# Kernel optimization log

Measured on AMD Instinct MI355X. Metric: run time of the kernel, lower is better.

The kernel has to match this reference:

```python
import jax, jax.numpy as jnp
import numpy as np

NUM_HEADS = 16
HEAD_DIM = 64  # hidden_size // num_heads


def _logsparse_allowed(seq_len):
    # allowed[i, j] True if key j is attended by query i:
    # j == i, j == i-1, or j == i - 2^k (k >= 1); combined with causal (j <= i).
    i = jnp.arange(seq_len)[:, None]
    j = jnp.arange(seq_len)[None, :]
    diff = i - j
    pow2 = (diff > 0) & ((diff & (diff - 1)) == 0)  # covers diff==1 and diff==2^k
    return (diff == 0) | pow2  # implies diff >= 0, so causal is subsumed


def setup_inputs() -> dict:
    key = jax.random.key(0)
    ks = jax.random.split(key, 7)
    B, S, H = 4, 2048, 1024
    return {
        "hidden_states": jax.random.normal(ks[0], (B, S, H), dtype=jnp.float32),
        "attention_mask": jnp.zeros((B, 1, 1, S), dtype=jnp.float32),
        "Wq": jax.random.normal(ks[1], (H, H), dtype=jnp.float32) * 0.02,
        "bq": jnp.zeros((H,), dtype=jnp.float32),
        "Wk": jax.random.normal(ks[2], (H, H), dtype=jnp.float32) * 0.02,
        "bk": jnp.zeros((H,), dtype=jnp.float32),
        "Wv": jax.random.normal(ks[3], (H, H), dtype=jnp.float32) * 0.02,
        "bv": jnp.zeros((H,), dtype=jnp.float32),
    }


def _split_heads(x):
    B, S, _ = x.shape
    return x.reshape(B, S, NUM_HEADS, HEAD_DIM).transpose(0, 2, 1, 3)  # b h t d


def reference(hidden_states, attention_mask, Wq, bq, Wk, bk, Wv, bv):
    B, S, H = hidden_states.shape
    q = _split_heads(hidden_states @ Wq.T + bq)
    k = _split_heads(hidden_states @ Wk.T + bk)
    v = _split_heads(hidden_states @ Wv.T + bv)

    scores = jnp.einsum("bhqd,bhkd->bhqk", q, k) * (HEAD_DIM ** -0.5)
    allowed = _logsparse_allowed(S)  # [S, S] bool
    scores = jnp.where(allowed[None, None], scores, -jnp.inf)
    scores = scores + attention_mask  # [B,1,1,S] additive mask
    probs = jax.nn.softmax(scores, axis=-1)
    out = jnp.einsum("bhqk,bhkd->bhqd", probs, v)
    return out.transpose(0, 2, 1, 3).reshape(B, S, H)
```

## Files before the change

kernel.cpp:

```cpp
#include <hip/hip_runtime.h>
#include <hip/hip_bf16.h>

#define S_LEN   2048
#define NHEADS  16
#define HDIM    64
#define HID     1024
#define BATCH   4
#define M_ROWS  (BATCH * S_LEN)

typedef __attribute__((ext_vector_type(8))) short short8;
typedef __attribute__((ext_vector_type(4))) float floatx4;
typedef __attribute__((ext_vector_type(4))) unsigned short ushort4v;

__device__ __forceinline__ unsigned short f2bf_rne(float x) {
  union { float f; unsigned u; } v; v.f = x;
  unsigned r = v.u + 0x7fffu + ((v.u >> 16) & 1u);
  return (unsigned short)(r >> 16);
}

__device__ __forceinline__ float bf2f(unsigned short u) {
  union { unsigned u; float f; } c; c.u = ((unsigned)u) << 16;
  return c.f;
}

__device__ __forceinline__ void glds16(const unsigned short* g, unsigned short* l) {
  __builtin_amdgcn_global_load_lds(
      (const __attribute__((address_space(1))) unsigned int*)g,
      (__attribute__((address_space(3))) unsigned int*)l, 16, 0, 0);
}

#define HS4 (M_ROWS * HID / 4)
#define W4  (HID * HID / 4)
__global__ __launch_bounds__(256) void cast_all(
    const float* __restrict__ hs, const float* __restrict__ Wq,
    const float* __restrict__ Wk, const float* __restrict__ Wv,
    unsigned short* __restrict__ hsb, unsigned short* __restrict__ wqb,
    unsigned short* __restrict__ wkb, unsigned short* __restrict__ wvb) {
  int idx = blockIdx.x * 256 + threadIdx.x;
  const float* in;
  unsigned short* out;
  int off;
  if (idx < HS4) {
    in = hs; out = hsb; off = idx;
  } else {
    int r = idx - HS4;
    int seg = r >> 18;
    off = r & (W4 - 1);
    in  = (seg == 0) ? Wq  : (seg == 1) ? Wk  : Wv;
    out = (seg == 0) ? wqb : (seg == 1) ? wkb : wvb;
  }
  floatx4 v = __builtin_nontemporal_load((const floatx4*)in + off);
  ushort4v o;
  o.x = f2bf_rne(v.x);
  o.y = f2bf_rne(v.y);
  o.z = f2bf_rne(v.z);
  o.w = f2bf_rne(v.w);
  ((ushort4v*)out)[off] = o;
}

__global__ __launch_bounds__(512, 2) void qkv_gemm(
    const unsigned short* __restrict__ A,
    const unsigned short* __restrict__ W0, const unsigned short* __restrict__ W1,
    const unsigned short* __restrict__ W2,
    const float* __restrict__ b0, const float* __restrict__ b1,
    const float* __restrict__ b2,
    unsigned short* __restrict__ O0, unsigned short* __restrict__ O1,
    unsigned short* __restrict__ O2) {
  const int K = HID;
  const int N = HID;

  __shared__ __align__(16) unsigned short lds[3 * 24576];

  const int tid = threadIdx.x;
  const int w = tid >> 6;
  const int lane = tid & 63;

  const int bid = blockIdx.x;
  const int xcd = bid & 7;
  const int rr  = bid >> 3;
  const int sb  = rr >> 5;
  const int q   = rr & 31;
  const int sbid = xcd * 3 + sb;
  const int mg = sbid & 7;
  const int sg = sbid >> 3;
  const int mi   = mg * 4 + (q & 3);
  const int slab = sg * 8 + (q >> 2);
  const int ni = slab & 7;
  const int z  = slab >> 3;
  const int m0 = mi << 8;
  const int n0 = ni << 7;

  const unsigned short* __restrict__ Wz = (z == 0) ? W0 : (z == 1) ? W1 : W2;
  const float* __restrict__ bias = (z == 0) ? b0 : (z == 1) ? b1 : b2;
  unsigned short* __restrict__ O = (z == 0) ? O0 : (z == 1) ? O1 : O2;

  const int lr = lane >> 3;
  const int ccs = (lane & 7) ^ lr;
  const unsigned short* gsrc[6];
  unsigned short* ldst[6];
  #pragma unroll
  for (int u = 0; u < 6; ++u) {
    const int seg = w * 6 + u;
    if (seg < 32) {
      gsrc[u] = A + (size_t)(m0 + seg * 8 + lr) * K + ccs * 8;
      ldst[u] = lds + seg * 512;
    } else {
      gsrc[u] = Wz + (size_t)(n0 + (seg - 32) * 8 + lr) * K + ccs * 8;
      ldst[u] = lds + 16384 + (seg - 32) * 512;
    }
  }

  auto stage3 = [&](int t, int h) {
    const int bofs = (t % 3) * 24576;
    const int ko = t * 64;
    #pragma unroll
    for (int u = h * 3; u < h * 3 + 3; ++u)
      glds16(gsrc[u] + ko, ldst[u] + bofs);
  };

  const int lrow = lane & 15;
  const int qd = lane >> 4;
  const int sw = lrow & 7;
  const int wm = w & 3;
  const int wn = w >> 2;
  const int arow = wm * 64 + lrow;
  const int brow = wn * 64 + lrow;

  floatx4 acc[4][4] = {};

  stage3(0, 0); stage3(0, 1);
  stage3(1, 0); stage3(1, 1);

  for (int t = 0; t < 16; ++t) {
    asm volatile("s_waitcnt lgkmcnt(0)" ::: "memory");
    if (t < 15) asm volatile("s_waitcnt vmcnt(6)" ::: "memory");
    else        asm volatile("s_waitcnt vmcnt(0)" ::: "memory");
    __builtin_amdgcn_s_barrier();
    asm volatile("" ::: "memory");

    const unsigned short* Asb = lds + (t % 3) * 24576;
    const unsigned short* Bsb = Asb + 16384;
    const bool pf = (t + 2 < 16);

    #pragma unroll
    for (int kk = 0; kk < 2; ++kk) {
      if (pf) stage3(t + 2, kk);
      const int cp = (((kk << 2) | qd) ^ sw) << 3;
      short8 af[4], bf[4];
      #pragma unroll
      for (int im = 0; im < 4; ++im)
        af[im] = *(const short8*)(Asb + (arow + im * 16) * 64 + cp);
      #pragma unroll
      for (int in = 0; in < 4; ++in)
        bf[in] = *(const short8*)(Bsb + (brow + in * 16) * 64 + cp);
      __builtin_amdgcn_s_setprio(1);
      #pragma unroll
      for (int im = 0; im < 4; ++im)
        #pragma unroll
        for (int in = 0; in < 4; ++in)
          acc[im][in] = __builtin_amdgcn_mfma_f32_16x16x32_bf16(af[im], bf[in], acc[im][in], 0, 0, 0);
      __builtin_amdgcn_s_setprio(0);
    }
  }

  #pragma unroll
  for (int im = 0; im < 4; ++im) {
    #pragma unroll
    for (int in = 0; in < 4; ++in) {
      const int col = n0 + wn * 64 + in * 16 + lrow;
      const float bb = bias[col];
      #pragma unroll
      for (int r = 0; r < 4; ++r) {
        const int row = m0 + wm * 64 + im * 16 + (qd << 2) + r;
        O[(size_t)row * N + col] = f2bf_rne(acc[im][in][r] + bb);
      }
    }
  }
}

__global__ __launch_bounds__(256) void logsparse_attn(
    const unsigned short* __restrict__ Q, const unsigned short* __restrict__ K,
    const unsigned short* __restrict__ V, const float* __restrict__ mask,
    float* __restrict__ out) {
  const int bid = (blockIdx.x & 7) * 512 + (blockIdx.x >> 3);
  const int tid = threadIdx.x;
  const int l = tid & 7;
  const int qglob = bid * 32 + (tid >> 3);

  const int i = qglob & (S_LEN - 1);
  const int h = (qglob >> 11) & (NHEADS - 1);
  const int b = qglob >> 15;

  const size_t base = (size_t)b * S_LEN * HID + h * HDIM + l * 8;

  int js[12];
  js[0] = i;
  int nj = 1;
  for (int d = 1; d <= i; d <<= 1) js[nj++] = i - d;
  #pragma unroll
  for (int t = 0; t < 12; ++t)
    if (t >= nj) js[t] = i;

  short8 k8[12];
  #pragma unroll
  for (int t = 0; t < 12; ++t)
    k8[t] = *(const short8*)(K + base + (size_t)js[t] * HID);
  const short8 q8 = *(const short8*)(Q + base + (size_t)i * HID);
  float mk[12];
  #pragma unroll
  for (int t = 0; t < 12; ++t)
    mk[t] = mask[b * S_LEN + js[t]];

  float qf[8];
  #pragma unroll
  for (int e = 0; e < 8; ++e) qf[e] = bf2f((unsigned short)q8[e]);

  float s[12];
  #pragma unroll
  for (int t = 0; t < 12; ++t) {
    float p = 0.f;
    #pragma unroll
    for (int e = 0; e < 8; ++e) p += qf[e] * bf2f((unsigned short)k8[t][e]);
    p += __shfl_xor(p, 1, 64);
    p += __shfl_xor(p, 2, 64);
    p += __shfl_xor(p, 4, 64);
    s[t] = (t < nj) ? (p * 0.125f + mk[t]) : -1e30f;
  }

  float mx = s[0];
  #pragma unroll
  for (int t = 1; t < 12; ++t) mx = fmaxf(mx, s[t]);
  float lsum = 0.f;
  #pragma unroll
  for (int t = 0; t < 12; ++t) { s[t] = __expf(s[t] - mx); lsum += s[t]; }
  const float inv = 1.f / lsum;

  short8 v8[12];
  #pragma unroll
  for (int t = 0; t < 12; ++t)
    v8[t] = *(const short8*)(V + base + (size_t)js[t] * HID);

  float o[8] = {};
  #pragma unroll
  for (int t = 0; t < 12; ++t) {
    #pragma unroll
    for (int e = 0; e < 8; ++e) o[e] += s[t] * bf2f((unsigned short)v8[t][e]);
  }

  float* op = out + base + (size_t)i * HID;
  floatx4 o0 = {o[0] * inv, o[1] * inv, o[2] * inv, o[3] * inv};
  floatx4 o1 = {o[4] * inv, o[5] * inv, o[6] * inv, o[7] * inv};
  __builtin_nontemporal_store(o0, (floatx4*)op);
  __builtin_nontemporal_store(o1, (floatx4*)(op + 4));
}

extern "C" void kernel_launch(void* const* d_in, const int* in_sizes, int n_in,
                              void* d_out, int out_size, void* d_ws, size_t ws_size,
                              hipStream_t stream) {
  const float* hs   = (const float*)d_in[0];
  const float* mask = (const float*)d_in[1];
  const float* Wq   = (const float*)d_in[2];
  const float* bq   = (const float*)d_in[3];
  const float* Wk   = (const float*)d_in[4];
  const float* bk   = (const float*)d_in[5];
  const float* Wv   = (const float*)d_in[6];
  const float* bv   = (const float*)d_in[7];
  float* out = (float*)d_out;

  unsigned short* hsb = (unsigned short*)d_ws;
  unsigned short* wqb = hsb + (size_t)M_ROWS * HID;
  unsigned short* wkb = wqb + (size_t)HID * HID;
  unsigned short* wvb = wkb + (size_t)HID * HID;
  unsigned short* Qb = wvb + (size_t)HID * HID;
  unsigned short* Kb = Qb + (size_t)M_ROWS * HID;
  unsigned short* Vb = Kb + (size_t)M_ROWS * HID;

  {
    int quads = HS4 + 3 * W4;
    cast_all<<<quads / 256, 256, 0, stream>>>(hs, Wq, Wk, Wv, hsb, wqb, wkb, wvb);
  }

  {
    qkv_gemm<<<768, 512, 0, stream>>>(hsb, wqb, wkb, wvb, bq, bk, bv, Qb, Kb, Vb);
  }

  {
    int blocks = (BATCH * NHEADS * S_LEN) / 32;
    logsparse_attn<<<blocks, 256, 0, stream>>>(Qb, Kb, Vb, mask, out);
  }
}
```

Before: 185.8 us.

## Enlarge QKV GEMM tile to 256x256 with BK=32 triple-buffered pipeline

Changes the fused QKV projection GEMM from 256x128 output tiles with a K-step of 64 to 256x256 tiles with a K-step of 32. Each wave now computes a 128x64 sub-tile, so more MFMAs run per LDS fragment load and global re-reads of A and W drop. The grid is halved to 384 blocks and the LDS swizzle and load mapping are reworked for 32-wide rows. The trade-offs are a larger accumulator register footprint, fewer blocks to fill the CUs, and twice as many barrier iterations.

Measured after the change: 183.9 us. No clear change (-1.1%).

```diff
diff --git a/kernel.cpp b/kernel.cpp
--- a/kernel.cpp
+++ b/kernel.cpp
@@ -69,7 +69,7 @@
   const int K = HID;
   const int N = HID;
 
-  __shared__ __align__(16) unsigned short lds[3 * 24576];
+  __shared__ __align__(16) unsigned short lds[3 * 16384];
 
   const int tid = threadIdx.x;
   const int w = tid >> 6;
@@ -78,100 +78,94 @@
   const int bid = blockIdx.x;
   const int xcd = bid & 7;
   const int rr  = bid >> 3;
-  const int sb  = rr >> 5;
-  const int q   = rr & 31;
-  const int sbid = xcd * 3 + sb;
+  const int sbl = rr >> 4;
+  const int q   = rr & 15;
+  const int sbid = xcd * 3 + sbl;
   const int mg = sbid & 7;
-  const int sg = sbid >> 3;
-  const int mi   = mg * 4 + (q & 3);
-  const int slab = sg * 8 + (q >> 2);
-  const int ni = slab & 7;
-  const int z  = slab >> 3;
+  const int z  = sbid >> 3;
+  const int mi = mg * 4 + (q & 3);
+  const int ni = q >> 2;
   const int m0 = mi << 8;
-  const int n0 = ni << 7;
+  const int n0 = ni << 8;
 
   const unsigned short* __restrict__ Wz = (z == 0) ? W0 : (z == 1) ? W1 : W2;
   const float* __restrict__ bias = (z == 0) ? b0 : (z == 1) ? b1 : b2;
   unsigned short* __restrict__ O = (z == 0) ? O0 : (z == 1) ? O1 : O2;
 
-  const int lr = lane >> 3;
-  const int ccs = (lane & 7) ^ lr;
-  const unsigned short* gsrc[6];
-  unsigned short* ldst[6];
-  #pragma unroll
-  for (int u = 0; u < 6; ++u) {
-    const int seg = w * 6 + u;
-    if (seg < 32) {
-      gsrc[u] = A + (size_t)(m0 + seg * 8 + lr) * K + ccs * 8;
-      ldst[u] = lds + seg * 512;
+  const int lr = lane >> 2;
+  const int gc = (lane & 3) ^ ((lr >> 1) & 3);
+  const unsigned short* gsrc[4];
+  unsigned short* ldst[4];
+  #pragma unroll
+  for (int u = 0; u < 4; ++u) {
+    const int seg = w * 4 + u;
+    if (seg < 16) {
+      gsrc[u] = A + (size_t)(m0 + seg * 16 + lr) * K + gc * 8;
     } else {
-      gsrc[u] = Wz + (size_t)(n0 + (seg - 32) * 8 + lr) * K + ccs * 8;
-      ldst[u] = lds + 16384 + (seg - 32) * 512;
+      gsrc[u] = Wz + (size_t)(n0 + (seg - 16) * 16 + lr) * K + gc * 8;
     }
-  }
-
-  auto stage3 = [&](int t, int h) {
-    const int bofs = (t % 3) * 24576;
-    const int ko = t * 64;
-    #pragma unroll
-    for (int u = h * 3; u < h * 3 + 3; ++u)
+    ldst[u] = lds + seg * 512;
+  }
+
+  auto stage = [&](int t) {
+    const int bofs = (t % 3) * 16384;
+    const int ko = t * 32;
+    #pragma unroll
+    for (int u = 0; u < 4; ++u)
       glds16(gsrc[u] + ko, ldst[u] + bofs);
   };
 
   const int lrow = lane & 15;
   const int qd = lane >> 4;
-  const int sw = lrow & 7;
-  const int wm = w & 3;
-  const int wn = w >> 2;
-  const int arow = wm * 64 + lrow;
+  const int cp = (qd ^ ((lrow >> 1) & 3)) * 8;
+  const int wm = w & 1;
+  const int wn = w >> 1;
+  const int arow = wm * 128 + lrow;
   const int brow = wn * 64 + lrow;
 
-  floatx4 acc[4][4] = {};
-
-  stage3(0, 0); stage3(0, 1);
-  stage3(1, 0); stage3(1, 1);
-
-  for (int t = 0; t < 16; ++t) {
+  floatx4 acc[8][4] = {};
+
+  stage(0);
+  stage(1);
+
+  for (int t = 0; t < 32; ++t) {
     asm volatile("s_waitcnt lgkmcnt(0)" ::: "memory");
-    if (t < 15) asm volatile("s_waitcnt vmcnt(6)" ::: "memory");
+    if (t < 31) asm volatile("s_waitcnt vmcnt(4)" ::: "memory");
     else        asm volatile("s_waitcnt vmcnt(0)" ::: "memory");
     __builtin_amdgcn_s_barrier();
     asm volatile("" ::: "memory");
 
-    const unsigned short* Asb = lds + (t % 3) * 24576;
-    const unsigned short* Bsb = Asb + 16384;
-    const bool pf = (t + 2 < 16);
-
-    #pragma unroll
-    for (int kk = 0; kk < 2; ++kk) {
-      if (pf) stage3(t + 2, kk);
-      const int cp = (((kk << 2) | qd) ^ sw) << 3;
-      short8 af[4], bf[4];
-      #pragma unroll
-      for (int im = 0; im < 4; ++im)
-        af[im] = *(const short8*)(Asb + (arow + im * 16) * 64 + cp);
+    const unsigned short* Asb = lds + (t % 3) * 16384;
+    const unsigned short* Bsb = Asb + 8192;
+
+    if (t + 2 < 32) stage(t + 2);
+
+    short8 af[8], bf[4];
+    #pragma unroll
+    for (int im = 0; im < 8; ++im)
+      af[im] = *(const short8*)(Asb + (arow + im * 16) * 32 + cp);
+    #pragma unroll
+    for (int in = 0; in < 4; ++in)
+      bf[in] = *(const short8*)(Bsb + (brow + in * 16) * 32 + cp);
+
+    __builtin_amdgcn_s_setprio(1);
+    #pragma unroll
+    for (int im = 0; im < 8; ++im)
       #pragma unroll
       for (int in = 0; in < 4; ++in)
-        bf[in] = *(const short8*)(Bsb + (brow + in * 16) * 64 + cp);
-      __builtin_amdgcn_s_setprio(1);
-      #pragma unroll
-      for (int im = 0; im < 4; ++im)
-        #pragma unroll
-        for (int in = 0; in < 4; ++in)
-          acc[im][in] = __builtin_amdgcn_mfma_f32_16x16x32_bf16(af[im], bf[in], acc[im][in], 0, 0, 0);
-      __builtin_amdgcn_s_setprio(0);
-    }
-  }
-
-  #pragma unroll
-  for (int im = 0; im < 4; ++im) {
+        acc[im][in] = __builtin_amdgcn_mfma_f32_16x16x32_bf16(af[im], bf[in], acc[im][in], 0, 0, 0);
+    __builtin_amdgcn_s_setprio(0);
+  }
+
+  #pragma unroll
+  for (int im = 0; im < 8; ++im) {
     #pragma unroll
     for (int in = 0; in < 4; ++in) {
       const int col = n0 + wn * 64 + in * 16 + lrow;
       const float bb = bias[col];
       #pragma unroll
       for (int r = 0; r < 4; ++r) {
-        const int row = m0 + wm * 64 + im * 16 + (qd << 2) + r;
+        const int row = m0 + wm * 128 + im * 16 + (qd << 2) + r;
         O[(size_t)row * N + col] = f2bf_rne(acc[im][in][r] + bb);
       }
     }
@@ -281,7 +275,7 @@
   }
 
   {
-    qkv_gemm<<<768, 512, 0, stream>>>(hsb, wqb, wkb, wvb, bq, bk, bv, Qb, Kb, Vb);
+    qkv_gemm<<<384, 512, 0, stream>>>(hsb, wqb, wkb, wvb, bq, bk, bv, Qb, Kb, Vb);
   }
 
   {
```
